# Kernel optimization log

Hardware: AMD Instinct MI355X
Metric: run time of the kernel (lower is better)

The kernel has to match this reference:

```python
import jax, jax.numpy as jnp
import numpy as np

B, L, H, E = 4, 2048, 8, 64
WINDOW = 8
DILATION = 1


def setup_inputs() -> dict:
    key = jax.random.key(0)
    kq, kk, kv, ka = jax.random.split(key, 4)
    queries = jax.random.normal(kq, (B, L, H, E), dtype=jnp.float32)
    keys = jax.random.normal(kk, (B, L, H, E), dtype=jnp.float32)
    values = jax.random.normal(kv, (B, L, H, E), dtype=jnp.float32)
    alpha = jax.random.uniform(ka, (1,), dtype=jnp.float32)
    return {"queries": queries, "keys": keys, "values": values, "alpha": alpha}


def _full_attention(q, k, v, scale):
    # q,k,v: [B, L, H, E]
    scores = jnp.einsum('blhe,bshe->bhls', q, k) * scale  # [B,H,L,L]
    A = jax.nn.softmax(scores, axis=-1)
    return jnp.einsum('bhls,bshd->blhd', A, v)


def _local_attention(q, k, v, scale):
    # efficient gather-based local window attention, non-causal
    Lk = k.shape[1]
    offsets = jnp.arange(-WINDOW, WINDOW + 1) * DILATION
    idx = jnp.clip(jnp.arange(Lk)[:, None] + offsets[None, :], 0, Lk - 1)
    K_win = k[:, idx]
    V_win = v[:, idx]
    scores = jnp.einsum('blhe,blwhe->blhw', q, K_win) * scale
    A = jax.nn.softmax(scores, axis=-1)
    return jnp.einsum('blhw,blwhe->blhe', A, V_win)


def reference(queries, keys, values, alpha):
    scale = 1.0 / np.sqrt(queries.shape[-1]).astype(np.float32)
    out_full = _full_attention(queries, keys, values, scale)
    out_local = _local_attention(queries, keys, values, scale)
    w = jax.nn.sigmoid(alpha[0])
    # only_target_first=True: positions 1..L-1 take out_full, position 0 is gated
    out = out_full.at[:, 0].set(w * out_full[:, 0] + (1.0 - w) * out_local[:, 0])
    return out
```

## Files before the change

### kernel.cpp

```cpp
#include <hip/hip_runtime.h>

typedef unsigned short u16;
typedef unsigned int   u32;
typedef __attribute__((ext_vector_type(8))) short short8;
typedef __attribute__((ext_vector_type(16))) float f32x16;

#define MFMA32(a, b, c) __builtin_amdgcn_mfma_f32_32x32x16_bf16(a, b, c, 0, 0, 0)

constexpr int Lv = 2048, Hv = 8, Ev = 64, HE = Hv * Ev;
constexpr float QSCALE = 0.18033688011112042f;

__device__ __forceinline__ float bf2f(u16 u) {
    u32 x = ((u32)u) << 16;
    return __builtin_bit_cast(float, x);
}
__device__ __forceinline__ u16 f2bf(float f) {
    u32 x = __builtin_bit_cast(u32, f);
    u32 r = ((x >> 16) & 1u) + 0x7fffu;
    return (u16)((x + r) >> 16);
}
__device__ __forceinline__ u32 pkbf(float a, float b) {
#if __has_builtin(__builtin_amdgcn_cvt_pk_bf16_f32)
    typedef __attribute__((ext_vector_type(2))) __bf16 bf16x2;
    bf16x2 v = __builtin_amdgcn_cvt_pk_bf16_f32(a, b);
    return __builtin_bit_cast(u32, v);
#else
    return (u32)f2bf(a) | ((u32)f2bf(b) << 16);
#endif
}
__device__ __forceinline__ float fexp2(float x) {
#if __has_builtin(__builtin_amdgcn_exp2f)
    return __builtin_amdgcn_exp2f(x);
#else
    return exp2f(x);
#endif
}

__device__ __forceinline__ int detect_isbf16(const u32* q32, int lane) {
    u32 w0 = q32[2 * lane];
    u32 w1 = q32[2 * lane + 1];
    u16 uu[4] = { (u16)(w0 & 0xffff), (u16)(w0 >> 16),
                  (u16)(w1 & 0xffff), (u16)(w1 >> 16) };
    int p = 0, z = 0;
#pragma unroll
    for (int j = 0; j < 4; ++j) {
        u16 mgn = (u16)(uu[j] & 0x7fff);
        int ex  = mgn >> 7;
        bool zero = (mgn == 0);
        bool pl   = zero || (ex >= 115 && ex <= 132);
        p += pl ? 1 : 0;
        if ((j & 1) == 0) z += zero ? 1 : 0;
    }
    int acc = p | (z << 16);
#pragma unroll
    for (int o = 1; o < 64; o <<= 1) acc += __shfl_xor(acc, o);
    int ps = acc & 0xffff, zs = acc >> 16;
    if (zs >= 100) return 0;
    return (ps >= 240) ? 1 : 0;
}

__device__ __forceinline__ short8 cvt8s(const float* p, float s) {
    float4 a = *(const float4*)p, b4 = *(const float4*)(p + 4);
    u32 r[4] = { pkbf(a.x * s, a.y * s), pkbf(a.z * s, a.w * s),
                 pkbf(b4.x * s, b4.y * s), pkbf(b4.z * s, b4.w * s) };
    return *(short8*)r;
}

__device__ __forceinline__ f32x16 zv16() {
    f32x16 z;
#pragma unroll
    for (int r = 0; r < 16; ++r) z[r] = 0.f;
    return z;
}

__device__ __forceinline__ void plswap(u32& a, u32& b) {
#if __has_builtin(__builtin_amdgcn_permlane32_swap)
    auto r = __builtin_amdgcn_permlane32_swap(a, b, false, false);
    a = r[0]; b = r[1];
#else
    int lane = (int)(threadIdx.x & 63);
    u32 ax = (u32)__shfl_xor((int)a, 32);
    u32 bx = (u32)__shfl_xor((int)b, 32);
    bool hi = lane >= 32;
    u32 na = hi ? bx : a;
    u32 nb = hi ? b  : ax;
    a = na; b = nb;
#endif
}

template <int ISBF>
__device__ __forceinline__ void attn_impl(
    const void* __restrict__ qv, const void* __restrict__ kv,
    const void* __restrict__ vv, const void* __restrict__ alphav,
    void* __restrict__ outv, u16* SMEM)
{
    const int tid  = threadIdx.x;
    const int w    = tid >> 6;
    const int lane = tid & 63;
    const int l31  = lane & 31;
    const int hi   = lane >> 5;
    const int qg   = w & 1;
    const int g    = w >> 1;
    const int t7   = tid & 127;

    const int fid = blockIdx.x;
    const int bh  = (fid & 7) * 4 + ((fid >> 3) & 3);
    const int rb  = fid >> 5;
    const int b   = bh >> 3, h = bh & 7;
    const int row0 = rb * 64;

    const size_t bhoff = (size_t)b * Lv * HE + h * Ev;
    const u16*   q16 = (const u16*)qv + bhoff;
    const u16*   k16 = (const u16*)kv + bhoff;
    const u16*   v16 = (const u16*)vv + bhoff;
    const float* q32 = (const float*)qv + bhoff;
    const float* k32 = (const float*)kv + bhoff;
    const float* v32 = (const float*)vv + bhoff;

    u16* Kg = SMEM + g * 4096;
    u16* Vg = SMEM + 8192 + g * 4096;

    short8 qf[4];
    {
        size_t ro = (size_t)(row0 + qg * 32 + l31) * HE + hi * 8;
        if (ISBF) {
#pragma unroll
            for (int c = 0; c < 4; ++c) {
                short8 t = *(const short8*)(q16 + ro + 16 * c);
#pragma unroll
                for (int j = 0; j < 8; ++j)
                    qf[c][j] = (short)f2bf(bf2f((u16)t[j]) * QSCALE);
            }
        } else {
#pragma unroll
            for (int c = 0; c < 4; ++c) qf[c] = cvt8s(q32 + ro + 16 * c, QSCALE);
        }
    }

    f32x16 O[2];
    O[0] = zv16(); O[1] = zv16();
    float psum = 0.f;

    const int kk0  = t7 >> 3, ks0 = t7 & 7;
    const int koff = kk0 * HE + ((ks0 ^ (kk0 & 7)) * 8);
    const int eq = t7 & 7, kp = t7 >> 3;
    const int kslot = kp >> 2, kpos = kp & 3;

    const size_t gkey = (size_t)g * 1024;

    float4 kfa, kfb, kfc, kfd, vfa, vfb, vfc, vfd;
    uint4  kru0, kru1, vru0, vru1;

#define LOAD_TILE(KT)                                                           \
    do {                                                                        \
        size_t kb_ = (gkey + (size_t)(KT) * 32) * HE;                           \
        if (ISBF) {                                                             \
            kru0 = *(const uint4*)(k16 + kb_ + koff);                           \
            kru1 = *(const uint4*)(k16 + kb_ + koff + 16 * HE);                 \
            const u16* vp_ = v16 + kb_ + (size_t)(2 * kp) * HE + eq * 8;        \
            vru0 = *(const uint4*)vp_;                                          \
            vru1 = *(const uint4*)(vp_ + HE);                                   \
        } else {                                                                \
            const float* kp_ = k32 + kb_ + koff;                                \
            kfa = *(const float4*)kp_;          kfb = *(const float4*)(kp_ + 4);\
            kfc = *(const float4*)(kp_ + 16 * HE);                              \
            kfd = *(const float4*)(kp_ + 16 * HE + 4);                          \
            const float* vp_ = v32 + kb_ + (size_t)(2 * kp) * HE + eq * 8;      \
            vfa = *(const float4*)vp_;          vfb = *(const float4*)(vp_ + 4);\
            vfc = *(const float4*)(vp_ + HE);   vfd = *(const float4*)(vp_ + HE + 4);\
        }                                                                       \
    } while (0)

#define STORE_TILE(KB, VB)                                                      \
    do {                                                                        \
        if (ISBF) {                                                             \
            *(uint4*)&(KB)[t7 * 8]         = kru0;                              \
            *(uint4*)&(KB)[(t7 + 128) * 8] = kru1;                              \
            const u16* a0_ = (const u16*)&vru0;                                 \
            const u16* a1_ = (const u16*)&vru1;                                 \
            _Pragma("unroll")                                                   \
            for (int j = 0; j < 8; ++j) {                                       \
                int e_  = eq * 8 + j;                                           \
                int sl_ = kslot ^ ((e_ + (e_ >> 3)) & 3);                       \
                u32 val_ = (u32)a0_[j] | ((u32)a1_[j] << 16);                   \
                *(u32*)&(VB)[e_ * 32 + sl_ * 8 + kpos * 2] = val_;              \
            }                                                                   \
        } else {                                                                \
            u32 k0_[4] = { pkbf(kfa.x, kfa.y), pkbf(kfa.z, kfa.w),              \
                           pkbf(kfb.x, kfb.y), pkbf(kfb.z, kfb.w) };            \
            u32 k1_[4] = { pkbf(kfc.x, kfc.y), pkbf(kfc.z, kfc.w),              \
                           pkbf(kfd.x, kfd.y), pkbf(kfd.z, kfd.w) };            \
            *(uint4*)&(KB)[t7 * 8]         = *(uint4*)k0_;                      \
            *(uint4*)&(KB)[(t7 + 128) * 8] = *(uint4*)k1_;                      \
            float t0_[8] = {vfa.x, vfa.y, vfa.z, vfa.w, vfb.x, vfb.y, vfb.z, vfb.w};\
            float t1_[8] = {vfc.x, vfc.y, vfc.z, vfc.w, vfd.x, vfd.y, vfd.z, vfd.w};\
            _Pragma("unroll")                                                   \
            for (int j = 0; j < 8; ++j) {                                       \
                int e_  = eq * 8 + j;                                           \
                int sl_ = kslot ^ ((e_ + (e_ >> 3)) & 3);                       \
                *(u32*)&(VB)[e_ * 32 + sl_ * 8 + kpos * 2] = pkbf(t0_[j], t1_[j]);\
            }                                                                   \
        }                                                                       \
    } while (0)

    LOAD_TILE(0);
    STORE_TILE(Kg, Vg);
    __syncthreads();

    for (int kt = 0; kt < 32; ++kt) {
        u16* Kb = Kg + (kt & 1) * 2048;
        u16* Vb = Vg + (kt & 1) * 2048;
        u16* Kn = Kg + ((kt & 1) ^ 1) * 2048;
        u16* Vn = Vg + ((kt & 1) ^ 1) * 2048;

        if (kt < 31) LOAD_TILE(kt + 1);

        f32x16 St = zv16();
#pragma unroll
        for (int c = 0; c < 4; ++c) {
            int sl = (2 * c + hi) ^ (l31 & 7);
            short8 kf = *(const short8*)&Kb[l31 * 64 + sl * 8];
            St = MFMA32(kf, qf[c], St);
        }

        float pe[16];
#pragma unroll
        for (int r = 0; r < 16; ++r) pe[r] = fexp2(St[r]);
#pragma unroll
        for (int r = 0; r < 16; ++r) psum += pe[r];
        u32 c8[8];
#pragma unroll
        for (int q = 0; q < 8; ++q) c8[q] = pkbf(pe[2 * q], pe[2 * q + 1]);
#pragma unroll
        for (int t = 0; t < 2; ++t) {
            u32 a0 = c8[4 * t + 0], a1 = c8[4 * t + 1];
            u32 a2 = c8[4 * t + 2], a3 = c8[4 * t + 3];
            plswap(a0, a2);
            plswap(a1, a3);
            u32 pw_[4] = { a0, a1, a2, a3 };
            short8 pa = *(short8*)pw_;
#pragma unroll
            for (int et = 0; et < 2; ++et) {
                int e  = et * 32 + l31;
                int sl = (2 * t + hi) ^ ((e + (e >> 3)) & 3);
                short8 vf = *(const short8*)&Vb[e * 32 + sl * 8];
                O[et] = MFMA32(pa, vf, O[et]);
            }
        }

        if (kt < 31) {
            STORE_TILE(Kn, Vn);
            __syncthreads();
        }
    }
#undef LOAD_TILE
#undef STORE_TILE

    __syncthreads();
    float pst = psum + __shfl_xor(psum, 32);
    float* cb = (float*)SMEM;
    const int cbase = qg * 2368 + lane * 36;

    if (g == 1) {
        union { f32x16 v; float4 q4[4]; } u;
        u.v = O[0];
#pragma unroll
        for (int i = 0; i < 4; ++i) *(float4*)&cb[cbase + 4 * i] = u.q4[i];
        u.v = O[1];
#pragma unroll
        for (int i = 0; i < 4; ++i) *(float4*)&cb[cbase + 16 + 4 * i] = u.q4[i];
        cb[qg * 2368 + 2304 + lane] = pst;
    }

    float locv[2] = {0.f, 0.f};
    float wgt = 0.f;
    const bool w0blk = (rb == 0) && (w == 0);
    if (w0blk) {
        const int e = lane;
        const size_t base = bhoff + e;
#define LDIN(p, i) (ISBF ? bf2f(((const u16*)(p))[i]) : ((const float*)(p))[i])
        float qe = LDIN(qv, base);
        float s[9];
#pragma unroll
        for (int j = 0; j < 9; ++j) {
            float prod = qe * LDIN(kv, base + (size_t)j * HE);
#pragma unroll
            for (int o = 1; o < 64; o <<= 1) prod += __shfl_xor(prod, o);
            s[j] = prod * 0.125f;
        }
        float mx = s[0];
#pragma unroll
        for (int j = 1; j < 9; ++j) mx = fmaxf(mx, s[j]);
        float we[9];
#pragma unroll
        for (int j = 0; j < 9; ++j) we[j] = expf(s[j] - mx);
        float denom = 9.f * we[0];
        float acc   = 9.f * we[0] * LDIN(vv, base);
#pragma unroll
        for (int j = 1; j < 9; ++j) {
            denom += we[j];
            acc   += we[j] * LDIN(vv, base + (size_t)j * HE);
        }
        float loc = acc / denom;

        float a;
        if (ISBF) {
            a = bf2f(((const u16*)alphav)[0]);
            if (!(a >= 0.0f && a <= 1.0f)) {
                float af = ((const float*)alphav)[0];
                if (af >= 0.0f && af <= 1.0f) a = af;
            }
        } else {
            a = ((const float*)alphav)[0];
            if (!(a >= 0.0f && a <= 1.0f)) {
                float ab = bf2f(((const u16*)alphav)[0]);
                if (ab >= 0.0f && ab <= 1.0f) a = ab;
            }
        }
        wgt = 1.f / (1.f + expf(-a));
#pragma unroll
        for (int et = 0; et < 2; ++et) locv[et] = __shfl(loc, et * 32 + l31);
#undef LDIN
    }

    __syncthreads();
    if (g != 0) return;

    float pstp = cb[qg * 2368 + 2304 + lane];
#pragma unroll
    for (int r = 0; r < 16; ++r) {
        O[0][r] += cb[cbase + r];
        O[1][r] += cb[cbase + 16 + r];
    }
    float invv = 1.0f / (pst + pstp);

#pragma unroll
    for (int rg = 0; rg < 4; ++rg) {
#pragma unroll
        for (int rr = 0; rr < 4; ++rr) {
            const int reg = rg * 4 + rr;
            const int rl  = rr + 8 * rg + 4 * hi;
            float inv = __shfl(invv, rl);
            int row = row0 + qg * 32 + rl;
            size_t oo = (size_t)(b * Lv + row) * HE + h * Ev + l31;
            bool blend = w0blk && (rl == 0);
#pragma unroll
            for (int et = 0; et < 2; ++et) {
                float res = O[et][reg] * inv;
                if (blend) res = wgt * res + (1.f - wgt) * locv[et];
                if (ISBF) ((u16*)outv)[oo + et * 32] = f2bf(res);
                else      ((float*)outv)[oo + et * 32] = res;
            }
        }
    }
}

__global__ __launch_bounds__(256, 4) void attn_kernel(
    const void* __restrict__ qv, const void* __restrict__ kv,
    const void* __restrict__ vv, const void* __restrict__ alphav,
    void* __restrict__ outv)
{
    __shared__ u16 SMEM[16384];

    const int isbf = detect_isbf16((const u32*)qv, threadIdx.x & 63);
    if (isbf) attn_impl<1>(qv, kv, vv, alphav, outv, SMEM);
    else      attn_impl<0>(qv, kv, vv, alphav, outv, SMEM);
}

extern "C" void kernel_launch(void* const* d_in, const int* in_sizes, int n_in,
                              void* d_out, int out_size, void* d_ws, size_t ws_size,
                              hipStream_t stream) {
    hipLaunchKernelGGL(attn_kernel, dim3(1024), dim3(256), 0, stream,
                       d_in[0], d_in[1], d_in[2], d_in[3], d_out);
}
```

Measured before the change: 162.1 us.

## Double query rows per block and share a 64-key K/V tile across split-K groups

```diff
diff --git a/kernel.cpp b/kernel.cpp
--- a/kernel.cpp
+++ b/kernel.cpp
@@ -99,15 +99,14 @@
     const int lane = tid & 63;
     const int l31  = lane & 31;
     const int hi   = lane >> 5;
-    const int qg   = w & 1;
-    const int g    = w >> 1;
-    const int t7   = tid & 127;
+    const int qg   = w & 3;
+    const int g    = w >> 2;
 
     const int fid = blockIdx.x;
     const int bh  = (fid & 7) * 4 + ((fid >> 3) & 3);
     const int rb  = fid >> 5;
     const int b   = bh >> 3, h = bh & 7;
-    const int row0 = rb * 64;
+    const int row0 = rb * 128;
 
     const size_t bhoff = (size_t)b * Lv * HE + h * Ev;
     const u16*   q16 = (const u16*)qv + bhoff;
@@ -117,8 +116,8 @@
     const float* k32 = (const float*)kv + bhoff;
     const float* v32 = (const float*)vv + bhoff;
 
-    u16* Kg = SMEM + g * 4096;
-    u16* Vg = SMEM + 8192 + g * 4096;
+    u16* Klds = SMEM;
+    u16* Vt   = SMEM + 8192;
 
     short8 qf[4];
     {
@@ -141,77 +140,69 @@
     O[0] = zv16(); O[1] = zv16();
     float psum = 0.f;
 
-    const int kk0  = t7 >> 3, ks0 = t7 & 7;
-    const int koff = kk0 * HE + ((ks0 ^ (kk0 & 7)) * 8);
-    const int eq = t7 & 7, kp = t7 >> 3;
-    const int kslot = kp >> 2, kpos = kp & 3;
-
-    const size_t gkey = (size_t)g * 1024;
-
-    float4 kfa, kfb, kfc, kfd, vfa, vfb, vfc, vfd;
-    uint4  kru0, kru1, vru0, vru1;
-
-#define LOAD_TILE(KT)                                                           \
-    do {                                                                        \
-        size_t kb_ = (gkey + (size_t)(KT) * 32) * HE;                           \
-        if (ISBF) {                                                             \
-            kru0 = *(const uint4*)(k16 + kb_ + koff);                           \
-            kru1 = *(const uint4*)(k16 + kb_ + koff + 16 * HE);                 \
-            const u16* vp_ = v16 + kb_ + (size_t)(2 * kp) * HE + eq * 8;        \
-            vru0 = *(const uint4*)vp_;                                          \
-            vru1 = *(const uint4*)(vp_ + HE);                                   \
-        } else {                                                                \
-            const float* kp_ = k32 + kb_ + koff;                                \
-            kfa = *(const float4*)kp_;          kfb = *(const float4*)(kp_ + 4);\
-            kfc = *(const float4*)(kp_ + 16 * HE);                              \
-            kfd = *(const float4*)(kp_ + 16 * HE + 4);                          \
-            const float* vp_ = v32 + kb_ + (size_t)(2 * kp) * HE + eq * 8;      \
-            vfa = *(const float4*)vp_;          vfb = *(const float4*)(vp_ + 4);\
-            vfc = *(const float4*)(vp_ + HE);   vfd = *(const float4*)(vp_ + HE + 4);\
-        }                                                                       \
+    const int kkey = tid >> 3, ksl = tid & 7;
+    const int koff = kkey * HE + ((ksl ^ (kkey & 7)) * 8);
+    const int eq = tid & 15, pp = tid >> 4;
+    const int kcv = pp >> 2, pq = pp & 3;
+
+    float4 kfa, kfb, vfa, vfb;
+    uint4  kru; uint2 vru0, vru1;
+
+#define LOAD_TILE(KT)                                                          \
+    do {                                                                       \
+        size_t kb_ = (size_t)(KT) * 64 * HE;                                   \
+        if (ISBF) {                                                            \
+            kru  = *(const uint4*)(k16 + kb_ + koff);                          \
+            const u16* vp_ = v16 + kb_ + (size_t)(2 * pp) * HE + eq * 4;       \
+            vru0 = *(const uint2*)vp_;                                         \
+            vru1 = *(const uint2*)(vp_ + HE);                                  \
+        } else {                                                               \
+            const float* kp_ = k32 + kb_ + koff;                               \
+            kfa = *(const float4*)kp_;                                         \
+            kfb = *(const float4*)(kp_ + 4);                                   \
+            const float* vp_ = v32 + kb_ + (size_t)(2 * pp) * HE + eq * 4;     \
+            vfa = *(const float4*)vp_;                                         \
+            vfb = *(const float4*)(vp_ + HE);                                  \
+        }                                                                      \
     } while (0)
 
-#define STORE_TILE(KB, VB)                                                      \
-    do {                                                                        \
-        if (ISBF) {                                                             \
-            *(uint4*)&(KB)[t7 * 8]         = kru0;                              \
-            *(uint4*)&(KB)[(t7 + 128) * 8] = kru1;                              \
-            const u16* a0_ = (const u16*)&vru0;                                 \
-            const u16* a1_ = (const u16*)&vru1;                                 \
-            _Pragma("unroll")                                                   \
-            for (int j = 0; j < 8; ++j) {                                       \
-                int e_  = eq * 8 + j;                                           \
-                int sl_ = kslot ^ ((e_ + (e_ >> 3)) & 3);                       \
-                u32 val_ = (u32)a0_[j] | ((u32)a1_[j] << 16);                   \
-                *(u32*)&(VB)[e_ * 32 + sl_ * 8 + kpos * 2] = val_;              \
-            }                                                                   \
-        } else {                                                                \
-            u32 k0_[4] = { pkbf(kfa.x, kfa.y), pkbf(kfa.z, kfa.w),              \
-                           pkbf(kfb.x, kfb.y), pkbf(kfb.z, kfb.w) };            \
-            u32 k1_[4] = { pkbf(kfc.x, kfc.y), pkbf(kfc.z, kfc.w),              \
-                           pkbf(kfd.x, kfd.y), pkbf(kfd.z, kfd.w) };            \
-            *(uint4*)&(KB)[t7 * 8]         = *(uint4*)k0_;                      \
-            *(uint4*)&(KB)[(t7 + 128) * 8] = *(uint4*)k1_;                      \
-            float t0_[8] = {vfa.x, vfa.y, vfa.z, vfa.w, vfb.x, vfb.y, vfb.z, vfb.w};\
-            float t1_[8] = {vfc.x, vfc.y, vfc.z, vfc.w, vfd.x, vfd.y, vfd.z, vfd.w};\
-            _Pragma("unroll")                                                   \
-            for (int j = 0; j < 8; ++j) {                                       \
-                int e_  = eq * 8 + j;                                           \
-                int sl_ = kslot ^ ((e_ + (e_ >> 3)) & 3);                       \
-                *(u32*)&(VB)[e_ * 32 + sl_ * 8 + kpos * 2] = pkbf(t0_[j], t1_[j]);\
-            }                                                                   \
-        }                                                                       \
+#define STORE_TILE(KB, VB)                                                     \
+    do {                                                                       \
+        if (ISBF) {                                                            \
+            *(uint4*)&(KB)[tid * 8] = kru;                                     \
+            const u16* a0_ = (const u16*)&vru0;                                \
+            const u16* a1_ = (const u16*)&vru1;                                \
+            _Pragma("unroll")                                                  \
+            for (int j = 0; j < 4; ++j) {                                      \
+                int e_  = eq * 4 + j;                                          \
+                int sl_ = kcv ^ ((e_ + (e_ >> 3)) & 7);                        \
+                u32 val_ = (u32)a0_[j] | ((u32)a1_[j] << 16);                  \
+                *(u32*)&(VB)[e_ * 64 + sl_ * 8 + pq * 2] = val_;               \
+            }                                                                  \
+        } else {                                                               \
+            u32 kk_[4] = { pkbf(kfa.x, kfa.y), pkbf(kfa.z, kfa.w),             \
+                           pkbf(kfb.x, kfb.y), pkbf(kfb.z, kfb.w) };           \
+            *(uint4*)&(KB)[tid * 8] = *(uint4*)kk_;                            \
+            float t0_[4] = {vfa.x, vfa.y, vfa.z, vfa.w};                       \
+            float t1_[4] = {vfb.x, vfb.y, vfb.z, vfb.w};                       \
+            _Pragma("unroll")                                                  \
+            for (int j = 0; j < 4; ++j) {                                      \
+                int e_  = eq * 4 + j;                                          \
+                int sl_ = kcv ^ ((e_ + (e_ >> 3)) & 7);                        \
+                *(u32*)&(VB)[e_ * 64 + sl_ * 8 + pq * 2] = pkbf(t0_[j], t1_[j]);\
+            }                                                                  \
+        }                                                                      \
     } while (0)
 
     LOAD_TILE(0);
-    STORE_TILE(Kg, Vg);
+    STORE_TILE(Klds, Vt);
     __syncthreads();
 
     for (int kt = 0; kt < 32; ++kt) {
-        u16* Kb = Kg + (kt & 1) * 2048;
-        u16* Vb = Vg + (kt & 1) * 2048;
-        u16* Kn = Kg + ((kt & 1) ^ 1) * 2048;
-        u16* Vn = Vg + ((kt & 1) ^ 1) * 2048;
+        u16* Kb = Klds + (kt & 1) * 4096;
+        u16* Vb = Vt   + (kt & 1) * 4096;
+        u16* Kn = Klds + ((kt & 1) ^ 1) * 4096;
+        u16* Vn = Vt   + ((kt & 1) ^ 1) * 4096;
 
         if (kt < 31) LOAD_TILE(kt + 1);
 
@@ -219,7 +210,7 @@
 #pragma unroll
         for (int c = 0; c < 4; ++c) {
             int sl = (2 * c + hi) ^ (l31 & 7);
-            short8 kf = *(const short8*)&Kb[l31 * 64 + sl * 8];
+            short8 kf = *(const short8*)&Kb[(g * 32 + l31) * 64 + sl * 8];
             St = MFMA32(kf, qf[c], St);
         }
 
@@ -239,11 +230,12 @@
             plswap(a1, a3);
             u32 pw_[4] = { a0, a1, a2, a3 };
             short8 pa = *(short8*)pw_;
+            int ks = 2 * g + t;
 #pragma unroll
             for (int et = 0; et < 2; ++et) {
                 int e  = et * 32 + l31;
-                int sl = (2 * t + hi) ^ ((e + (e >> 3)) & 3);
-                short8 vf = *(const short8*)&Vb[e * 32 + sl * 8];
+                int sl = (2 * ks + hi) ^ ((e + (e >> 3)) & 7);
+                short8 vf = *(const short8*)&Vb[e * 64 + sl * 8];
                 O[et] = MFMA32(pa, vf, O[et]);
             }
         }
@@ -355,12 +347,12 @@
     }
 }
 
-__global__ __launch_bounds__(256, 4) void attn_kernel(
+__global__ __launch_bounds__(512, 4) void attn_kernel(
     const void* __restrict__ qv, const void* __restrict__ kv,
     const void* __restrict__ vv, const void* __restrict__ alphav,
     void* __restrict__ outv)
 {
-    __shared__ u16 SMEM[16384];
+    __shared__ u16 SMEM[18944];
 
     const int isbf = detect_isbf16((const u32*)qv, threadIdx.x & 63);
     if (isbf) attn_impl<1>(qv, kv, vv, alphav, outv, SMEM);
@@ -370,6 +362,6 @@
 extern "C" void kernel_launch(void* const* d_in, const int* in_sizes, int n_in,
                               void* d_out, int out_size, void* d_ws, size_t ws_size,
                               hipStream_t stream) {
-    hipLaunchKernelGGL(attn_kernel, dim3(1024), dim3(256), 0, stream,
+    hipLaunchKernelGGL(attn_kernel, dim3(512), dim3(512), 0, stream,
                        d_in[0], d_in[1], d_in[2], d_in[3], d_out);
 }
```

Measured after the change: 146.5 us. -9.6%, faster.
